# Kernel tuning notes

Hardware: AMD Instinct MI355X
Metric: run time of the kernel (lower is better)

Reference implementation:

```python
import jax, jax.numpy as jnp
import numpy as np

N = 50000      # total nodes
G = 100        # graphs in batch
NPG = N // G   # nodes per graph (contiguous)
E = 800000     # total edges (avg degree 16)
F_IN = 256
HID = 128
C = 4


def setup_inputs() -> dict:
    key = jax.random.key(0)
    ks = jax.random.split(key, 16)
    w = lambda k, shape: (jax.random.normal(k, shape, dtype=jnp.float32) * 0.02)
    x = jax.random.normal(ks[0], (N, F_IN), dtype=jnp.float32)
    # edges within graphs: pick a graph per edge, then local src/dst
    g = jax.random.randint(ks[1], (E,), 0, G, dtype=jnp.int32)
    src = g * NPG + jax.random.randint(ks[2], (E,), 0, NPG, dtype=jnp.int32)
    dst = g * NPG + jax.random.randint(ks[3], (E,), 0, NPG, dtype=jnp.int32)
    edge_index = jnp.stack([src, dst], axis=0)
    batch = jnp.repeat(jnp.arange(G, dtype=jnp.int32), NPG)
    return {
        "x": x,
        "edge_index": edge_index,
        "batch": batch,
        "num_graphs": G,
        "W_bu1": w(ks[4], (F_IN, HID)), "b_bu1": jnp.zeros((HID,), jnp.float32),
        "W_td1": w(ks[5], (F_IN, HID)), "b_td1": jnp.zeros((HID,), jnp.float32),
        "W_bu2": w(ks[6], (F_IN + HID, HID)), "b_bu2": jnp.zeros((HID,), jnp.float32),
        "W_td2": w(ks[7], (F_IN + HID, HID)), "b_td2": jnp.zeros((HID,), jnp.float32),
        "W_lin": w(ks[8], (2 * HID, C)), "b_lin": jnp.zeros((C,), jnp.float32),
    }


def _gcn(h_in, src, dst, W, b, n):
    """PyG GCNConv: sym-normalized aggregation with self loops, then bias."""
    h = h_in @ W                                        # [N, H]
    # deg = in-degree at dst + 1 (self loop)
    deg = jnp.ones((n,), h.dtype).at[dst].add(jnp.ones(src.shape, h.dtype))
    dinv = jax.lax.rsqrt(deg)                           # [N]
    coef = (dinv[src] * dinv[dst])[:, None]             # [E, 1]
    agg = jnp.zeros_like(h).at[dst].add(h[src] * coef)  # scatter-add messages
    agg = agg + h * (dinv * dinv)[:, None]              # self-loop term
    return agg + b


def reference(x, edge_index, batch, num_graphs,
              W_bu1, b_bu1, W_td1, b_td1,
              W_bu2, b_bu2, W_td2, b_td2,
              W_lin, b_lin):
    n = x.shape[0]
    g = num_graphs
    src, dst = edge_index[0], edge_index[1]  # top-down direction
    # root = first node index of each (contiguous) graph
    root = jax.ops.segment_min(jnp.arange(n), batch, num_segments=g)  # [G]
    root_full = x[root][batch]                                        # repeat_interleave of root feats
    # layer 1: bottom-up uses flipped edges, top-down uses edges as-is
    l1_bu = _gcn(x, dst, src, W_bu1, b_bu1, n)
    l1_td = _gcn(x, src, dst, W_td1, b_td1, n)
    cb = jax.nn.relu(jnp.concatenate([root_full, l1_bu], axis=-1))  # dropout is identity in eval
    ct = jax.nn.relu(jnp.concatenate([root_full, l1_td], axis=-1))
    # layer 2: original code passes the top-down edge_index to BOTH convs
    l2_bu = jax.nn.relu(_gcn(cb, src, dst, W_bu2, b_bu2, n))
    l2_td = jax.nn.relu(_gcn(ct, src, dst, W_td2, b_td2, n))
    # repeat root rows over each graph then segment-mean == the root row itself
    pb = l2_bu[root]   # [G, HID]
    pt = l2_td[root]   # [G, HID]
    total = jnp.concatenate([pb, pt], axis=-1)          # [G, 2*HID]
    return jax.nn.log_softmax(total @ W_lin + b_lin, axis=-1)
```

## Files before the change

### kernel.cpp

```cpp
#include <hip/hip_runtime.h>
#include <math.h>

constexpr int F_IN = 256;
constexpr int HID  = 128;
constexpr int CLS  = 4;

constexpr int SMAX  = 2560;
constexpr int ECAP  = 64;
constexpr int QCAP  = 512;
constexpr int GMAX  = 128;
constexpr int NXCD  = 8;

__device__ __forceinline__ int xcc_id() {
  int x;
  asm volatile("s_getreg_b32 %0, hwreg(HW_REG_XCC_ID)" : "=s"(x));
  return x & (NXCD - 1);
}

__device__ __forceinline__ int degsum(const int* __restrict__ cnt, int N, int v) {
  int d = 0;
#pragma unroll
  for (int k = 0; k < NXCD; ++k) d += cnt[k * N + v];
  return d;
}

__global__ void k_setup(int* __restrict__ sidx, int* __restrict__ slist,
                        int* __restrict__ counters,
                        int* __restrict__ cnt_bu, int* __restrict__ cnt_td,
                        int* __restrict__ qcur, int* __restrict__ cur_bu,
                        int* __restrict__ cur_td, int N, int G, int NPG) {
  int i = blockIdx.x * blockDim.x + threadIdx.x;
  if (i == 0) counters[0] = G;
  if (i < GMAX) qcur[i] = 0;
  if (i < SMAX) { cur_bu[i] = 0; cur_td[i] = 0; }
  if (i >= N) return;
#pragma unroll
  for (int k = 0; k < NXCD; ++k) { cnt_bu[k * N + i] = 0; cnt_td[k * N + i] = 0; }
  int g = i / NPG;
  bool isroot = (i - g * NPG) == 0;
  sidx[i] = isroot ? g : -1;
  if (isroot) slist[g] = i;
}

__global__ void k_claim(const int* __restrict__ src, const int* __restrict__ dst,
                        int* __restrict__ sidx, int* __restrict__ slist,
                        int* __restrict__ qbuf, int* __restrict__ qcur,
                        int* __restrict__ counters, int E, int NPG) {
  int i = blockIdx.x * blockDim.x + threadIdx.x;
  int e0 = i * 4;
  int dv[4];
  int ne = 0;
  if (e0 + 3 < E) {
    int4 d4 = ((const int4*)dst)[i];
    dv[0] = d4.x; dv[1] = d4.y; dv[2] = d4.z; dv[3] = d4.w;
    ne = 4;
  } else {
    for (int e = e0; e < E; ++e) dv[ne++] = dst[e];
  }
#pragma unroll
  for (int k = 0; k < 4; ++k) {
    if (k >= ne) break;
    int d = dv[k];
    int dg = d / NPG;
    if (d - dg * NPG == 0) {
      int s = src[e0 + k];
      int p = atomicAdd(&qcur[dg], 1);
      if (p < QCAP) qbuf[dg * QCAP + p] = s;
      if (atomicCAS(&sidx[s], -1, -2) == -1) {
        int slot = atomicAdd(&counters[0], 1);
        if (slot < SMAX) { slist[slot] = s; sidx[s] = slot; }
        else sidx[s] = -1;
      }
    }
  }
}

__global__ void k_degfill(const int* __restrict__ src, const int* __restrict__ dst,
                          const int* __restrict__ sidx,
                          int* __restrict__ cnt_bu, int* __restrict__ cnt_td,
                          int* __restrict__ cur_bu, int* __restrict__ cur_td,
                          int* __restrict__ ebuf_bu, int* __restrict__ ebuf_td,
                          int E, int N) {
  int xc = xcc_id();
  int* cb = cnt_bu + xc * N;
  int* ct = cnt_td + xc * N;
  int i = blockIdx.x * blockDim.x + threadIdx.x;
  int e0 = i * 4;
  int sv[4], dv[4];
  int ne = 0;
  if (e0 + 3 < E) {
    int4 s4 = ((const int4*)src)[i];
    int4 d4 = ((const int4*)dst)[i];
    sv[0] = s4.x; sv[1] = s4.y; sv[2] = s4.z; sv[3] = s4.w;
    dv[0] = d4.x; dv[1] = d4.y; dv[2] = d4.z; dv[3] = d4.w;
    ne = 4;
  } else {
    for (int e = e0; e < E; ++e) { sv[ne] = src[e]; dv[ne] = dst[e]; ++ne; }
  }
#pragma unroll
  for (int k = 0; k < 4; ++k) {
    if (k >= ne) break;
    int s = sv[k], d = dv[k];
    __hip_atomic_fetch_add(&cb[s], 1, __ATOMIC_RELAXED, __HIP_MEMORY_SCOPE_WORKGROUP);
    __hip_atomic_fetch_add(&ct[d], 1, __ATOMIC_RELAXED, __HIP_MEMORY_SCOPE_WORKGROUP);
    int ss = sidx[s];
    if (ss >= 0) { int p = atomicAdd(&cur_bu[ss], 1); if (p < ECAP) ebuf_bu[ss * ECAP + p] = d; }
    int sd = sidx[d];
    if (sd >= 0) { int p = atomicAdd(&cur_td[sd], 1); if (p < ECAP) ebuf_td[sd * ECAP + p] = s; }
  }
}

__global__ __launch_bounds__(256) void k_gl1(
    const float* __restrict__ x, const int* __restrict__ slist,
    const int* __restrict__ counters,
    const int* __restrict__ cnt_bu, const int* __restrict__ cnt_td,
    const int* __restrict__ ebuf_bu, const int* __restrict__ ebuf_td,
    const float* __restrict__ Wbu, const float* __restrict__ bbu,
    const float* __restrict__ Wtd, const float* __restrict__ btd,
    float* __restrict__ l1_bu, float* __restrict__ l1_td, int N) {
  constexpr int TS = 8;
  __shared__ float zb[TS][F_IN];
  __shared__ float zt[TS][F_IN];
  int scnt = min(counters[0], SMAX);
  int base = blockIdx.x * TS;
  if (base >= scnt) return;
  int ns = min(TS, scnt - base);
  int tid = threadIdx.x, lane = tid & 63, wv = tid >> 6;
  for (int q = 0; q < 4; ++q) {
    int unit = wv * 4 + q;
    int sl = unit & 7;
    bool td = unit >= 8;
    if (sl >= ns) continue;
    const int* cnt = td ? cnt_td : cnt_bu;
    const int* eb  = (td ? ebuf_td : ebuf_bu) + (base + sl) * ECAP;
    int u = slist[base + sl];
    int dg = degsum(cnt, N, u);
    int m = min(dg, ECAP);
    float ax = 0.f, ay = 0.f, az = 0.f, aw = 0.f;
    for (int j = 0; j < m; ++j) {
      int node = eb[j];
      float dv = rsqrtf(1.f + (float)degsum(cnt, N, node));
      float4 v = ((const float4*)x)[(size_t)node * 64 + lane];
      ax += dv * v.x; ay += dv * v.y; az += dv * v.z; aw += dv * v.w;
    }
    float du = rsqrtf(1.f + (float)dg);
    float4 xv = ((const float4*)x)[(size_t)u * 64 + lane];
    float* zrow = td ? zt[sl] : zb[sl];
    zrow[lane * 4 + 0] = du * ax + du * du * xv.x;
    zrow[lane * 4 + 1] = du * ay + du * du * xv.y;
    zrow[lane * 4 + 2] = du * az + du * du * xv.z;
    zrow[lane * 4 + 3] = du * aw + du * du * xv.w;
  }
  __syncthreads();
  bool isbu = (tid < HID);
  int h = isbu ? tid : tid - HID;
  const float* W = isbu ? Wbu : Wtd;
  float acc[TS];
#pragma unroll
  for (int t = 0; t < TS; ++t) acc[t] = 0.f;
  for (int f = 0; f < F_IN; ++f) {
    float wvv = W[f * HID + h];
#pragma unroll
    for (int t = 0; t < TS; ++t) acc[t] += (isbu ? zb[t][f] : zt[t][f]) * wvv;
  }
  float bias = isbu ? bbu[h] : btd[h];
  float* outp = isbu ? l1_bu : l1_td;
  for (int t = 0; t < ns; ++t)
    outp[(size_t)(base + t) * HID + h] = acc[t] + bias;
}

__global__ void k_out(const float* __restrict__ x,
                      const int* __restrict__ sidx, const int* __restrict__ cnt_td,
                      const int* __restrict__ qbuf, const int* __restrict__ qcur,
                      const float* __restrict__ l1_bu, const float* __restrict__ l1_td,
                      const float* __restrict__ Wbu2, const float* __restrict__ bbu2,
                      const float* __restrict__ Wtd2, const float* __restrict__ btd2,
                      const float* __restrict__ Wlin, const float* __restrict__ blin,
                      float* __restrict__ out, int G, int NPG, int N) {
  __shared__ int   s_slot[QCAP + 1];
  __shared__ float s_coef[QCAP + 1];
  __shared__ float front[F_IN];
  __shared__ float av[2 * HID];
  __shared__ float total[2 * HID];
  __shared__ float logits[CLS];
  int g = blockIdx.x;
  int tid = threadIdx.x;
  int r = g * NPG;
  int nq = min(qcur[g], QCAP);
  int items = nq + 1;
  float dr = rsqrtf(1.f + (float)degsum(cnt_td, N, r));
  for (int i = tid; i < items; i += 256) {
    int s = (i < nq) ? qbuf[g * QCAP + i] : r;
    s_slot[i] = sidx[s];
    s_coef[i] = rsqrtf(1.f + (float)degsum(cnt_td, N, s)) * dr;
  }
  __syncthreads();
  bool isbu = (tid < HID);
  int h = isbu ? tid : tid - HID;
  const float* l1v = isbu ? l1_bu : l1_td;
  float acc = 0.f, csum = 0.f;
  for (int i = 0; i < items; ++i) {
    float c = s_coef[i];
    csum += c;
    int slot = s_slot[i];
    if (slot >= 0) acc += c * fmaxf(l1v[(size_t)slot * HID + h], 0.f);
  }
  av[tid]    = acc;
  front[tid] = csum * fmaxf(x[(size_t)r * F_IN + tid], 0.f);
  __syncthreads();
  const float* W  = isbu ? Wbu2 : Wtd2;
  const float* ah = isbu ? av : (av + HID);
  float acc2 = isbu ? bbu2[h] : btd2[h];
  for (int f = 0; f < F_IN; ++f) acc2 += front[f] * W[f * HID + h];
  for (int j = 0; j < HID; ++j)  acc2 += ah[j] * W[(F_IN + j) * HID + h];
  total[tid] = fmaxf(acc2, 0.f);
  __syncthreads();
  if (tid < CLS) {
    float a = blin[tid];
    for (int k = 0; k < 2 * HID; ++k) a += total[k] * Wlin[k * CLS + tid];
    logits[tid] = a;
  }
  __syncthreads();
  if (tid < CLS) {
    float m = logits[0];
    for (int c = 1; c < CLS; ++c) m = fmaxf(m, logits[c]);
    float se = 0.f;
    for (int c = 0; c < CLS; ++c) se += expf(logits[c] - m);
    out[(size_t)g * CLS + tid] = logits[tid] - m - logf(se);
  }
}

extern "C" void kernel_launch(void* const* d_in, const int* in_sizes, int n_in,
                              void* d_out, int out_size, void* d_ws, size_t ws_size,
                              hipStream_t stream) {
  const float* x    = (const float*)d_in[0];
  const int*  eidx  = (const int*)d_in[1];
  const float* Wbu1 = (const float*)d_in[4];
  const float* bbu1 = (const float*)d_in[5];
  const float* Wtd1 = (const float*)d_in[6];
  const float* btd1 = (const float*)d_in[7];
  const float* Wbu2 = (const float*)d_in[8];
  const float* bbu2 = (const float*)d_in[9];
  const float* Wtd2 = (const float*)d_in[10];
  const float* btd2 = (const float*)d_in[11];
  const float* Wlin = (const float*)d_in[12];
  const float* blin = (const float*)d_in[13];
  float* out = (float*)d_out;

  int N = in_sizes[2];
  int E = in_sizes[1] / 2;
  int G = out_size / CLS;
  int NPG = N / G;
  const int* src = eidx;
  const int* dst = eidx + E;

  char* p = (char*)d_ws;
  auto alloc = [&](size_t bytes) -> char* {
    char* r = p; p += (bytes + 255) & ~(size_t)255; return r;
  };
  int*   counters  = (int*)  alloc(64);
  int*   cnt_bu    = (int*)  alloc((size_t)NXCD * N * 4);
  int*   cnt_td    = (int*)  alloc((size_t)NXCD * N * 4);
  int*   qcur      = (int*)  alloc((size_t)GMAX * 4);
  int*   cur_bu    = (int*)  alloc((size_t)SMAX * 4);
  int*   cur_td    = (int*)  alloc((size_t)SMAX * 4);
  int*   sidx      = (int*)  alloc((size_t)N * 4);
  int*   slist     = (int*)  alloc((size_t)SMAX * 4);
  int*   qbuf      = (int*)  alloc((size_t)GMAX * QCAP * 4);
  int*   ebuf_bu   = (int*)  alloc((size_t)SMAX * ECAP * 4);
  int*   ebuf_td   = (int*)  alloc((size_t)SMAX * ECAP * 4);
  float* l1_bu     = (float*)alloc((size_t)SMAX * HID * 4);
  float* l1_td     = (float*)alloc((size_t)SMAX * HID * 4);

  const int T = 256;
  int quarter = (E + 3) / 4;
  k_setup  <<<(N + T - 1) / T, T, 0, stream>>>(sidx, slist, counters,
                                               cnt_bu, cnt_td, qcur, cur_bu, cur_td,
                                               N, G, NPG);
  k_claim  <<<(quarter + T - 1) / T, T, 0, stream>>>(src, dst, sidx, slist,
                                                     qbuf, qcur, counters, E, NPG);
  k_degfill<<<(quarter + T - 1) / T, T, 0, stream>>>(src, dst, sidx,
                                                     cnt_bu, cnt_td, cur_bu, cur_td,
                                                     ebuf_bu, ebuf_td, E, N);
  k_gl1    <<<(SMAX + 7) / 8, T, 0, stream>>>(x, slist, counters, cnt_bu, cnt_td,
                                              ebuf_bu, ebuf_td,
                                              Wbu1, bbu1, Wtd1, btd1, l1_bu, l1_td, N);
  k_out    <<<G, T, 0, stream>>>(x, sidx, cnt_td, qbuf, qcur,
                                 l1_bu, l1_td, Wbu2, bbu2, Wtd2, btd2,
                                 Wlin, blin, out, G, NPG, N);
}
```

Baseline: 284.8 us.

## Drop per-XCD degree counters and widen layer-1 gather block to 1024 threads

Removes the per-XCD privatized degree count arrays and uses a single device-scope atomic counter per node. Degree reads in the layer-1 gather and the output kernel then need one load instead of eight. The layer-1 kernel now runs 1024 threads per block, giving one wave per (seed, direction) unit instead of four units per wave. Each thread also computes two output rows instead of eight in the small matmul. The cost is more contention from device-scope atomics in degfill and possibly lower occupancy from the larger blocks.

```diff
diff --git a/kernel.cpp b/kernel.cpp
--- a/kernel.cpp
+++ b/kernel.cpp
@@ -9,20 +9,6 @@
 constexpr int ECAP  = 64;
 constexpr int QCAP  = 512;
 constexpr int GMAX  = 128;
-constexpr int NXCD  = 8;
-
-__device__ __forceinline__ int xcc_id() {
-  int x;
-  asm volatile("s_getreg_b32 %0, hwreg(HW_REG_XCC_ID)" : "=s"(x));
-  return x & (NXCD - 1);
-}
-
-__device__ __forceinline__ int degsum(const int* __restrict__ cnt, int N, int v) {
-  int d = 0;
-#pragma unroll
-  for (int k = 0; k < NXCD; ++k) d += cnt[k * N + v];
-  return d;
-}
 
 __global__ void k_setup(int* __restrict__ sidx, int* __restrict__ slist,
                         int* __restrict__ counters,
@@ -34,8 +20,8 @@
   if (i < GMAX) qcur[i] = 0;
   if (i < SMAX) { cur_bu[i] = 0; cur_td[i] = 0; }
   if (i >= N) return;
-#pragma unroll
-  for (int k = 0; k < NXCD; ++k) { cnt_bu[k * N + i] = 0; cnt_td[k * N + i] = 0; }
+  cnt_bu[i] = 0;
+  cnt_td[i] = 0;
   int g = i / NPG;
   bool isroot = (i - g * NPG) == 0;
   sidx[i] = isroot ? g : -1;
@@ -80,10 +66,7 @@
                           int* __restrict__ cnt_bu, int* __restrict__ cnt_td,
                           int* __restrict__ cur_bu, int* __restrict__ cur_td,
                           int* __restrict__ ebuf_bu, int* __restrict__ ebuf_td,
-                          int E, int N) {
-  int xc = xcc_id();
-  int* cb = cnt_bu + xc * N;
-  int* ct = cnt_td + xc * N;
+                          int E) {
   int i = blockIdx.x * blockDim.x + threadIdx.x;
   int e0 = i * 4;
   int sv[4], dv[4];
@@ -101,8 +84,8 @@
   for (int k = 0; k < 4; ++k) {
     if (k >= ne) break;
     int s = sv[k], d = dv[k];
-    __hip_atomic_fetch_add(&cb[s], 1, __ATOMIC_RELAXED, __HIP_MEMORY_SCOPE_WORKGROUP);
-    __hip_atomic_fetch_add(&ct[d], 1, __ATOMIC_RELAXED, __HIP_MEMORY_SCOPE_WORKGROUP);
+    atomicAdd(&cnt_bu[s], 1);
+    atomicAdd(&cnt_td[d], 1);
     int ss = sidx[s];
     if (ss >= 0) { int p = atomicAdd(&cur_bu[ss], 1); if (p < ECAP) ebuf_bu[ss * ECAP + p] = d; }
     int sd = sidx[d];
@@ -110,14 +93,14 @@
   }
 }
 
-__global__ __launch_bounds__(256) void k_gl1(
+__global__ __launch_bounds__(1024) void k_gl1(
     const float* __restrict__ x, const int* __restrict__ slist,
     const int* __restrict__ counters,
     const int* __restrict__ cnt_bu, const int* __restrict__ cnt_td,
     const int* __restrict__ ebuf_bu, const int* __restrict__ ebuf_td,
     const float* __restrict__ Wbu, const float* __restrict__ bbu,
     const float* __restrict__ Wtd, const float* __restrict__ btd,
-    float* __restrict__ l1_bu, float* __restrict__ l1_td, int N) {
+    float* __restrict__ l1_bu, float* __restrict__ l1_td) {
   constexpr int TS = 8;
   __shared__ float zb[TS][F_IN];
   __shared__ float zt[TS][F_IN];
@@ -126,47 +109,49 @@
   if (base >= scnt) return;
   int ns = min(TS, scnt - base);
   int tid = threadIdx.x, lane = tid & 63, wv = tid >> 6;
-  for (int q = 0; q < 4; ++q) {
-    int unit = wv * 4 + q;
-    int sl = unit & 7;
-    bool td = unit >= 8;
-    if (sl >= ns) continue;
-    const int* cnt = td ? cnt_td : cnt_bu;
-    const int* eb  = (td ? ebuf_td : ebuf_bu) + (base + sl) * ECAP;
-    int u = slist[base + sl];
-    int dg = degsum(cnt, N, u);
-    int m = min(dg, ECAP);
-    float ax = 0.f, ay = 0.f, az = 0.f, aw = 0.f;
-    for (int j = 0; j < m; ++j) {
-      int node = eb[j];
-      float dv = rsqrtf(1.f + (float)degsum(cnt, N, node));
-      float4 v = ((const float4*)x)[(size_t)node * 64 + lane];
-      ax += dv * v.x; ay += dv * v.y; az += dv * v.z; aw += dv * v.w;
+  {
+    int sl = wv & 7;
+    bool td = wv >= 8;
+    if (sl < ns) {
+      const int* cnt = td ? cnt_td : cnt_bu;
+      const int* eb  = (td ? ebuf_td : ebuf_bu) + (base + sl) * ECAP;
+      int u = slist[base + sl];
+      int dg = cnt[u];
+      int m = min(dg, ECAP);
+      float ax = 0.f, ay = 0.f, az = 0.f, aw = 0.f;
+      for (int j = 0; j < m; ++j) {
+        int node = eb[j];
+        float dv = rsqrtf(1.f + (float)cnt[node]);
+        float4 v = ((const float4*)x)[(size_t)node * 64 + lane];
+        ax += dv * v.x; ay += dv * v.y; az += dv * v.z; aw += dv * v.w;
+      }
+      float du = rsqrtf(1.f + (float)dg);
+      float4 xv = ((const float4*)x)[(size_t)u * 64 + lane];
+      float* zrow = td ? zt[sl] : zb[sl];
+      zrow[lane * 4 + 0] = du * ax + du * du * xv.x;
+      zrow[lane * 4 + 1] = du * ay + du * du * xv.y;
+      zrow[lane * 4 + 2] = du * az + du * du * xv.z;
+      zrow[lane * 4 + 3] = du * aw + du * du * xv.w;
     }
-    float du = rsqrtf(1.f + (float)dg);
-    float4 xv = ((const float4*)x)[(size_t)u * 64 + lane];
-    float* zrow = td ? zt[sl] : zb[sl];
-    zrow[lane * 4 + 0] = du * ax + du * du * xv.x;
-    zrow[lane * 4 + 1] = du * ay + du * du * xv.y;
-    zrow[lane * 4 + 2] = du * az + du * du * xv.z;
-    zrow[lane * 4 + 3] = du * aw + du * du * xv.w;
-  }
-  __syncthreads();
-  bool isbu = (tid < HID);
-  int h = isbu ? tid : tid - HID;
+  }
+  __syncthreads();
+  int h256 = tid & 255;
+  int sgrp = tid >> 8;
+  bool isbu = (h256 < HID);
+  int h = isbu ? h256 : h256 - HID;
   const float* W = isbu ? Wbu : Wtd;
-  float acc[TS];
-#pragma unroll
-  for (int t = 0; t < TS; ++t) acc[t] = 0.f;
+  const float (*Z)[F_IN] = isbu ? zb : zt;
+  int t0 = sgrp * 2, t1 = sgrp * 2 + 1;
+  float a0 = 0.f, a1 = 0.f;
   for (int f = 0; f < F_IN; ++f) {
     float wvv = W[f * HID + h];
-#pragma unroll
-    for (int t = 0; t < TS; ++t) acc[t] += (isbu ? zb[t][f] : zt[t][f]) * wvv;
+    a0 += Z[t0][f] * wvv;
+    a1 += Z[t1][f] * wvv;
   }
   float bias = isbu ? bbu[h] : btd[h];
   float* outp = isbu ? l1_bu : l1_td;
-  for (int t = 0; t < ns; ++t)
-    outp[(size_t)(base + t) * HID + h] = acc[t] + bias;
+  if (t0 < ns) outp[(size_t)(base + t0) * HID + h] = a0 + bias;
+  if (t1 < ns) outp[(size_t)(base + t1) * HID + h] = a1 + bias;
 }
 
 __global__ void k_out(const float* __restrict__ x,
@@ -176,7 +161,7 @@
                       const float* __restrict__ Wbu2, const float* __restrict__ bbu2,
                       const float* __restrict__ Wtd2, const float* __restrict__ btd2,
                       const float* __restrict__ Wlin, const float* __restrict__ blin,
-                      float* __restrict__ out, int G, int NPG, int N) {
+                      float* __restrict__ out, int G, int NPG) {
   __shared__ int   s_slot[QCAP + 1];
   __shared__ float s_coef[QCAP + 1];
   __shared__ float front[F_IN];
@@ -188,11 +173,11 @@
   int r = g * NPG;
   int nq = min(qcur[g], QCAP);
   int items = nq + 1;
-  float dr = rsqrtf(1.f + (float)degsum(cnt_td, N, r));
+  float dr = rsqrtf(1.f + (float)cnt_td[r]);
   for (int i = tid; i < items; i += 256) {
     int s = (i < nq) ? qbuf[g * QCAP + i] : r;
     s_slot[i] = sidx[s];
-    s_coef[i] = rsqrtf(1.f + (float)degsum(cnt_td, N, s)) * dr;
+    s_coef[i] = rsqrtf(1.f + (float)cnt_td[s]) * dr;
   }
   __syncthreads();
   bool isbu = (tid < HID);
@@ -259,8 +244,8 @@
     char* r = p; p += (bytes + 255) & ~(size_t)255; return r;
   };
   int*   counters  = (int*)  alloc(64);
-  int*   cnt_bu    = (int*)  alloc((size_t)NXCD * N * 4);
-  int*   cnt_td    = (int*)  alloc((size_t)NXCD * N * 4);
+  int*   cnt_bu    = (int*)  alloc((size_t)N * 4);
+  int*   cnt_td    = (int*)  alloc((size_t)N * 4);
   int*   qcur      = (int*)  alloc((size_t)GMAX * 4);
   int*   cur_bu    = (int*)  alloc((size_t)SMAX * 4);
   int*   cur_td    = (int*)  alloc((size_t)SMAX * 4);
@@ -281,11 +266,11 @@
                                                      qbuf, qcur, counters, E, NPG);
   k_degfill<<<(quarter + T - 1) / T, T, 0, stream>>>(src, dst, sidx,
                                                      cnt_bu, cnt_td, cur_bu, cur_td,
-                                                     ebuf_bu, ebuf_td, E, N);
-  k_gl1    <<<(SMAX + 7) / 8, T, 0, stream>>>(x, slist, counters, cnt_bu, cnt_td,
-                                              ebuf_bu, ebuf_td,
-                                              Wbu1, bbu1, Wtd1, btd1, l1_bu, l1_td, N);
+                                                     ebuf_bu, ebuf_td, E);
+  k_gl1    <<<(SMAX + 7) / 8, 1024, 0, stream>>>(x, slist, counters, cnt_bu, cnt_td,
+                                                 ebuf_bu, ebuf_td,
+                                                 Wbu1, bbu1, Wtd1, btd1, l1_bu, l1_td);
   k_out    <<<G, T, 0, stream>>>(x, sidx, cnt_td, qbuf, qcur,
                                  l1_bu, l1_td, Wbu2, bbu2, Wtd2, btd2,
-                                 Wlin, blin, out, G, NPG, N);
-}
+                                 Wlin, blin, out, G, NPG);
+}
```

New measurement: 254.0 us. -10.8%, faster.
